# Performance work log

Hardware: AMD Instinct MI355X
Metric: run time of the kernel (lower is better)

The kernel has to match this reference:

```python
import jax, jax.numpy as jnp
import numpy as np


def setup_inputs() -> dict:
    key = jax.random.key(0)
    k1, k2, k3 = jax.random.split(key, 3)
    B, S, D = 8, 1024, 128
    logits = jax.random.normal(k1, (B, S, D), dtype=jnp.float32)
    labels = jax.random.normal(k2, (B, S, D), dtype=jnp.float32)
    # all-valid mask: any fully-padded row would make the softmax row all -inf (NaN),
    # matching the original torch behavior; ones keeps the baseline finite.
    pad_mask = jnp.ones((B, S), dtype=jnp.int32)
    ad_idxs = jax.random.randint(k3, (B, S), 0, 1000, dtype=jnp.int64)
    return {"logits": logits, "labels": labels, "pad_mask": pad_mask, "ad_idxs": ad_idxs}


def reference(logits, labels, pad_mask, ad_idxs):
    B, S, D = logits.shape
    N = B * S
    logits_flat = logits.reshape(N, D)
    labels_flat = labels.reshape(N, D)
    valid = pad_mask.reshape(N).astype(bool)
    ad = ad_idxs.reshape(N)

    # [N, N] pairwise similarity
    sim = logits_flat @ labels_flat.T
    pair_valid = valid[:, None] & valid[None, :]
    sim = jnp.where(pair_valid, sim, -jnp.inf)

    sim_prob = jax.nn.softmax(sim, axis=-1)

    label_mat = ((ad[:, None] == ad[None, :]) & pair_valid).astype(sim_prob.dtype)
    EPS = 1e-12
    pos_loss = -jnp.log2(jnp.clip(sim_prob, EPS)) * label_mat
    loss = pos_loss.sum(axis=-1).mean()
    return loss
```

## Files before the change

### kernel.cpp

```cpp
#include <hip/hip_runtime.h>
#include <math.h>

#define N 8192
#define D 128
#define NCHUNK 32
#define CHUNK_COLS (N / NCHUNK)
#define MAXPOS 32
#define NBUCKET 1000

#define CLIP_TERM 39.86313713864835f
#define LOG2E     1.4426950408889634f

typedef short bf16x8 __attribute__((ext_vector_type(8)));
typedef float f32x4  __attribute__((ext_vector_type(4)));

static __device__ __forceinline__ unsigned short f2bf(float f) {
    unsigned u = __builtin_bit_cast(unsigned, f);
    u += 0x7FFFu + ((u >> 16) & 1u);
    return (unsigned short)(u >> 16);
}

static __device__ __forceinline__ float exp2_fast(float x) {
    return __builtin_amdgcn_exp2f(x);
}

__global__ void convert_kernel(const float* __restrict__ a,
                               const float* __restrict__ b,
                               uint4* __restrict__ A,
                               uint4* __restrict__ B,
                               const int* __restrict__ ad,
                               int* __restrict__ bcnt,
                               int* __restrict__ blist,
                               int* __restrict__ cnt,
                               float* __restrict__ l_total,
                               float* __restrict__ out) {
    const int t = blockIdx.x * 256 + threadIdx.x;
    if (t < N) {
        cnt[t] = 0; l_total[t] = 0.0f;
        const int bv = ad[t];
        const int slot = atomicAdd(&bcnt[bv], 1);
        if (slot < MAXPOS) blist[bv * MAXPOS + slot] = t;
    }
    if (t == 0) *out = 0.0f;
    const int half = N * D / 8;
    const bool first = t < half;
    const int u = first ? t : t - half;
    const int r = u >> 4, k8 = u & 15;
    const float4* src = first ? (const float4*)a : (const float4*)b;
    float4 v0 = src[u * 2], v1 = src[u * 2 + 1];
    if (first) {
        v0.x *= LOG2E; v0.y *= LOG2E; v0.z *= LOG2E; v0.w *= LOG2E;
        v1.x *= LOG2E; v1.y *= LOG2E; v1.z *= LOG2E; v1.w *= LOG2E;
    }
    union { unsigned short us[8]; uint4 v; } p;
    p.us[0] = f2bf(v0.x); p.us[1] = f2bf(v0.y); p.us[2] = f2bf(v0.z); p.us[3] = f2bf(v0.w);
    p.us[4] = f2bf(v1.x); p.us[5] = f2bf(v1.y); p.us[6] = f2bf(v1.z); p.us[7] = f2bf(v1.w);
    const int chunk = ((r >> 4) * 4 + (k8 >> 2)) * 64 + (k8 & 3) * 16 + (r & 15);
    (first ? A : B)[chunk] = p.v;
}

__global__ __launch_bounds__(256, 2)
void sim_lse_kernel(const uint4* __restrict__ Ach,
                    const uint4* __restrict__ Bch,
                    float* __restrict__ l_total) {
    const int tid = threadIdx.x;
    const int lane = tid & 63;
    const int w = tid >> 6;
    const int quad = lane >> 4;
    const int rowBase = blockIdx.x * 256 + w * 64;
    const int col0 = blockIdx.y * CHUNK_COLS;
    const int rtile0 = rowBase >> 4;

    bf16x8 afr[4][4];
#pragma unroll
    for (int rt = 0; rt < 4; ++rt)
#pragma unroll
        for (int kt = 0; kt < 4; ++kt)
            afr[rt][kt] = __builtin_bit_cast(bf16x8,
                Ach[((rtile0 + rt) * 4 + kt) * 64 + lane]);

    float l[16];
#pragma unroll
    for (int s = 0; s < 16; ++s) l[s] = 0.0f;

#pragma unroll 2
    for (int cs = 0; cs < CHUNK_COLS / 32; ++cs) {
        const int ctile0 = (col0 >> 4) + cs * 2;

        bf16x8 bfr[2][4];
#pragma unroll
        for (int ct = 0; ct < 2; ++ct)
#pragma unroll
            for (int kt = 0; kt < 4; ++kt)
                bfr[ct][kt] = __builtin_bit_cast(bf16x8,
                    Bch[((ctile0 + ct) * 4 + kt) * 64 + lane]);

        f32x4 acc[4][2];
#pragma unroll
        for (int rt = 0; rt < 4; ++rt) { acc[rt][0] = (f32x4)(0.0f); acc[rt][1] = (f32x4)(0.0f); }

#pragma unroll
        for (int kt = 0; kt < 4; ++kt)
#pragma unroll
            for (int rt = 0; rt < 4; ++rt) {
                acc[rt][0] = __builtin_amdgcn_mfma_f32_16x16x32_bf16(afr[rt][kt], bfr[0][kt], acc[rt][0], 0, 0, 0);
                acc[rt][1] = __builtin_amdgcn_mfma_f32_16x16x32_bf16(afr[rt][kt], bfr[1][kt], acc[rt][1], 0, 0, 0);
            }

#pragma unroll
        for (int rt = 0; rt < 4; ++rt)
#pragma unroll
            for (int reg = 0; reg < 4; ++reg)
                l[rt * 4 + reg] += exp2_fast(acc[rt][0][reg]) + exp2_fast(acc[rt][1][reg]);
    }

#pragma unroll
    for (int s = 0; s < 16; ++s) {
        float ls = l[s];
#pragma unroll
        for (int off = 1; off < 16; off <<= 1) ls += __shfl_xor(ls, off, 64);
        if ((lane & 15) == 0) {
            const int rg = rowBase + (s >> 2) * 16 + quad * 4 + (s & 3);
            atomicAdd(&l_total[rg], ls);
        }
    }
}

__global__ __launch_bounds__(256)
void pos_pair_kernel(const float* __restrict__ logits,
                     const float* __restrict__ labels,
                     const int* __restrict__ bcnt,
                     const int* __restrict__ blist,
                     int* __restrict__ cnt,
                     float* __restrict__ pos_sim) {
    __shared__ float4 Lg[MAXPOS * 32];
    __shared__ float4 Lb[MAXPOS * 32];
    __shared__ int rows[MAXPOS];
    const int bId = blockIdx.x;
    const int nb = min(bcnt[bId], MAXPOS);
    const int tid = threadIdx.x;
    if (tid < nb) rows[tid] = blist[bId * MAXPOS + tid];
    __syncthreads();
    for (int idx = tid; idx < nb * 32; idx += 256) {
        const int rl = idx >> 5, c = idx & 31;
        const int rg = rows[rl];
        Lg[rl * 32 + c] = ((const float4*)logits)[rg * 32 + c];
        Lb[rl * 32 + c] = ((const float4*)labels)[rg * 32 + c];
    }
    __syncthreads();
    const int pairs = nb * nb;
    for (int p = tid; p < pairs; p += 256) {
        const int i = p / nb, j = p - i * nb;
        float sx = 0.f, sy = 0.f, sz = 0.f, sw = 0.f;
#pragma unroll 8
        for (int c = 0; c < 32; ++c) {
            const float4 x = Lg[i * 32 + c];
            const float4 y = Lb[j * 32 + c];
            sx = fmaf(x.x, y.x, sx); sy = fmaf(x.y, y.y, sy);
            sz = fmaf(x.z, y.z, sz); sw = fmaf(x.w, y.w, sw);
        }
        const float t = ((sx + sy) + (sz + sw)) * LOG2E;
        const int rg = rows[i];
        const int slot = atomicAdd(&cnt[rg], 1);
        if (slot < MAXPOS) pos_sim[rg * MAXPOS + slot] = t;
    }
}

__global__ __launch_bounds__(256)
void finalize_kernel(const float* __restrict__ l_total,
                     const int* __restrict__ cnt,
                     const float* __restrict__ pos_sim,
                     float* __restrict__ out) {
    const int i = blockIdx.x * 256 + threadIdx.x;
    const float lse = log2f(l_total[i]);
    const int n = min(cnt[i], MAXPOS);
    float sum = 0.0f;
    for (int k = 0; k < n; ++k)
        sum += fminf(lse - pos_sim[i * MAXPOS + k], CLIP_TERM);

#pragma unroll
    for (int off = 32; off >= 1; off >>= 1) sum += __shfl_xor(sum, off, 64);
    __shared__ float red[4];
    const int lane = threadIdx.x & 63, wid = threadIdx.x >> 6;
    if (lane == 0) red[wid] = sum;
    __syncthreads();
    if (threadIdx.x == 0)
        atomicAdd(out, (red[0] + red[1] + red[2] + red[3]) * (1.0f / (float)N));
}

extern "C" void kernel_launch(void* const* d_in, const int* in_sizes, int n_in,
                              void* d_out, int out_size, void* d_ws, size_t ws_size,
                              hipStream_t stream) {
    const float* logits = (const float*)d_in[0];
    const float* labels = (const float*)d_in[1];
    const int* ad = (const int*)d_in[3];
    float* out = (float*)d_out;

    uint4* Ach = (uint4*)d_ws;
    uint4* Bch = Ach + N * D / 8;
    float* l_total = (float*)(Bch + N * D / 8);
    int* cnt = (int*)(l_total + N);
    float* pos_sim = (float*)(cnt + N);
    int* bcnt = (int*)(pos_sim + N * MAXPOS);
    int* blist = bcnt + NBUCKET;

    hipMemsetAsync(bcnt, 0, NBUCKET * sizeof(int), stream);
    convert_kernel<<<2 * N * D / 8 / 256, 256, 0, stream>>>(
        logits, labels, Ach, Bch, ad, bcnt, blist, cnt, l_total, out);
    dim3 g(N / 256, NCHUNK);
    sim_lse_kernel<<<g, 256, 0, stream>>>(Ach, Bch, l_total);
    pos_pair_kernel<<<NBUCKET, 256, 0, stream>>>(logits, labels, bcnt, blist, cnt, pos_sim);
    finalize_kernel<<<N / 256, 256, 0, stream>>>(l_total, cnt, pos_sim, out);
}
```

Baseline: 107.0 us.

## Merge convert and positive-pair kernels, replace atomics with per-chunk partials

Folds the bf16 conversion and the positive-pair dot products into one prep kernel, where each bucket block scans all ad indices itself. This removes the memset, the bucket-list atomics and one kernel launch. The LSE accumulation switches from atomicAdd on l_total to writing per-chunk partial sums that finalize reduces. This avoids both atomic contention and the need to zero the buffer. In exchange, each of the 1000 bucket blocks reads the full 8192-entry index array, which adds redundant global reads.

Result: slower. 110.7 us (+3.4%).

```diff
diff --git a/kernel.cpp b/kernel.cpp
--- a/kernel.cpp
+++ b/kernel.cpp
@@ -24,123 +24,55 @@
     return __builtin_amdgcn_exp2f(x);
 }
 
-__global__ void convert_kernel(const float* __restrict__ a,
-                               const float* __restrict__ b,
-                               uint4* __restrict__ A,
-                               uint4* __restrict__ B,
-                               const int* __restrict__ ad,
-                               int* __restrict__ bcnt,
-                               int* __restrict__ blist,
-                               int* __restrict__ cnt,
-                               float* __restrict__ l_total,
-                               float* __restrict__ out) {
-    const int t = blockIdx.x * 256 + threadIdx.x;
-    if (t < N) {
-        cnt[t] = 0; l_total[t] = 0.0f;
-        const int bv = ad[t];
-        const int slot = atomicAdd(&bcnt[bv], 1);
-        if (slot < MAXPOS) blist[bv * MAXPOS + slot] = t;
-    }
-    if (t == 0) *out = 0.0f;
-    const int half = N * D / 8;
-    const bool first = t < half;
-    const int u = first ? t : t - half;
-    const int r = u >> 4, k8 = u & 15;
-    const float4* src = first ? (const float4*)a : (const float4*)b;
-    float4 v0 = src[u * 2], v1 = src[u * 2 + 1];
-    if (first) {
-        v0.x *= LOG2E; v0.y *= LOG2E; v0.z *= LOG2E; v0.w *= LOG2E;
-        v1.x *= LOG2E; v1.y *= LOG2E; v1.z *= LOG2E; v1.w *= LOG2E;
-    }
-    union { unsigned short us[8]; uint4 v; } p;
-    p.us[0] = f2bf(v0.x); p.us[1] = f2bf(v0.y); p.us[2] = f2bf(v0.z); p.us[3] = f2bf(v0.w);
-    p.us[4] = f2bf(v1.x); p.us[5] = f2bf(v1.y); p.us[6] = f2bf(v1.z); p.us[7] = f2bf(v1.w);
-    const int chunk = ((r >> 4) * 4 + (k8 >> 2)) * 64 + (k8 & 3) * 16 + (r & 15);
-    (first ? A : B)[chunk] = p.v;
-}
-
-__global__ __launch_bounds__(256, 2)
-void sim_lse_kernel(const uint4* __restrict__ Ach,
-                    const uint4* __restrict__ Bch,
-                    float* __restrict__ l_total) {
+__global__ __launch_bounds__(256)
+void prep_kernel(const float* __restrict__ logits,
+                 const float* __restrict__ labels,
+                 const int* __restrict__ ad,
+                 uint4* __restrict__ Ach,
+                 uint4* __restrict__ Bch,
+                 int* __restrict__ cnt,
+                 float* __restrict__ pos_sim,
+                 float* __restrict__ out) {
     const int tid = threadIdx.x;
-    const int lane = tid & 63;
-    const int w = tid >> 6;
-    const int quad = lane >> 4;
-    const int rowBase = blockIdx.x * 256 + w * 64;
-    const int col0 = blockIdx.y * CHUNK_COLS;
-    const int rtile0 = rowBase >> 4;
-
-    bf16x8 afr[4][4];
-#pragma unroll
-    for (int rt = 0; rt < 4; ++rt)
-#pragma unroll
-        for (int kt = 0; kt < 4; ++kt)
-            afr[rt][kt] = __builtin_bit_cast(bf16x8,
-                Ach[((rtile0 + rt) * 4 + kt) * 64 + lane]);
-
-    float l[16];
-#pragma unroll
-    for (int s = 0; s < 16; ++s) l[s] = 0.0f;
-
-#pragma unroll 2
-    for (int cs = 0; cs < CHUNK_COLS / 32; ++cs) {
-        const int ctile0 = (col0 >> 4) + cs * 2;
-
-        bf16x8 bfr[2][4];
-#pragma unroll
-        for (int ct = 0; ct < 2; ++ct)
-#pragma unroll
-            for (int kt = 0; kt < 4; ++kt)
-                bfr[ct][kt] = __builtin_bit_cast(bf16x8,
-                    Bch[((ctile0 + ct) * 4 + kt) * 64 + lane]);
-
-        f32x4 acc[4][2];
-#pragma unroll
-        for (int rt = 0; rt < 4; ++rt) { acc[rt][0] = (f32x4)(0.0f); acc[rt][1] = (f32x4)(0.0f); }
-
-#pragma unroll
-        for (int kt = 0; kt < 4; ++kt)
-#pragma unroll
-            for (int rt = 0; rt < 4; ++rt) {
-                acc[rt][0] = __builtin_amdgcn_mfma_f32_16x16x32_bf16(afr[rt][kt], bfr[0][kt], acc[rt][0], 0, 0, 0);
-                acc[rt][1] = __builtin_amdgcn_mfma_f32_16x16x32_bf16(afr[rt][kt], bfr[1][kt], acc[rt][1], 0, 0, 0);
-            }
-
-#pragma unroll
-        for (int rt = 0; rt < 4; ++rt)
-#pragma unroll
-            for (int reg = 0; reg < 4; ++reg)
-                l[rt * 4 + reg] += exp2_fast(acc[rt][0][reg]) + exp2_fast(acc[rt][1][reg]);
-    }
-
-#pragma unroll
-    for (int s = 0; s < 16; ++s) {
-        float ls = l[s];
-#pragma unroll
-        for (int off = 1; off < 16; off <<= 1) ls += __shfl_xor(ls, off, 64);
-        if ((lane & 15) == 0) {
-            const int rg = rowBase + (s >> 2) * 16 + quad * 4 + (s & 3);
-            atomicAdd(&l_total[rg], ls);
-        }
-    }
-}
-
-__global__ __launch_bounds__(256)
-void pos_pair_kernel(const float* __restrict__ logits,
-                     const float* __restrict__ labels,
-                     const int* __restrict__ bcnt,
-                     const int* __restrict__ blist,
-                     int* __restrict__ cnt,
-                     float* __restrict__ pos_sim) {
+
+    if (blockIdx.x < 2 * N * D / 8 / 256) {
+        const int t = blockIdx.x * 256 + tid;
+        if (t == 0) *out = 0.0f;
+        const int half = N * D / 8;
+        const bool first = t < half;
+        const int u = first ? t : t - half;
+        const int r = u >> 4, k8 = u & 15;
+        const float4* src = first ? (const float4*)logits : (const float4*)labels;
+        float4 v0 = src[u * 2], v1 = src[u * 2 + 1];
+        if (first) {
+            v0.x *= LOG2E; v0.y *= LOG2E; v0.z *= LOG2E; v0.w *= LOG2E;
+            v1.x *= LOG2E; v1.y *= LOG2E; v1.z *= LOG2E; v1.w *= LOG2E;
+        }
+        union { unsigned short us[8]; uint4 v; } p;
+        p.us[0] = f2bf(v0.x); p.us[1] = f2bf(v0.y); p.us[2] = f2bf(v0.z); p.us[3] = f2bf(v0.w);
+        p.us[4] = f2bf(v1.x); p.us[5] = f2bf(v1.y); p.us[6] = f2bf(v1.z); p.us[7] = f2bf(v1.w);
+        const int chunk = ((r >> 4) * 4 + (k8 >> 2)) * 64 + (k8 & 3) * 16 + (r & 15);
+        (first ? Ach : Bch)[chunk] = p.v;
+        return;
+    }
+
     __shared__ float4 Lg[MAXPOS * 32];
     __shared__ float4 Lb[MAXPOS * 32];
     __shared__ int rows[MAXPOS];
-    const int bId = blockIdx.x;
-    const int nb = min(bcnt[bId], MAXPOS);
-    const int tid = threadIdx.x;
-    if (tid < nb) rows[tid] = blist[bId * MAXPOS + tid];
-    __syncthreads();
+    __shared__ int nbs;
+    const int bId = blockIdx.x - 2 * N * D / 8 / 256;
+    if (tid == 0) nbs = 0;
+    __syncthreads();
+    for (int r = tid; r < N; r += 256) {
+        if (ad[r] == bId) {
+            const int s = atomicAdd(&nbs, 1);
+            if (s < MAXPOS) rows[s] = r;
+            else cnt[r] = 0;
+        }
+    }
+    __syncthreads();
+    const int nb = min(nbs, MAXPOS);
+    if (tid < nb) cnt[rows[tid]] = nb;
     for (int idx = tid; idx < nb * 32; idx += 256) {
         const int rl = idx >> 5, c = idx & 31;
         const int rg = rows[rl];
@@ -159,20 +91,91 @@
             sx = fmaf(x.x, y.x, sx); sy = fmaf(x.y, y.y, sy);
             sz = fmaf(x.z, y.z, sz); sw = fmaf(x.w, y.w, sw);
         }
-        const float t = ((sx + sy) + (sz + sw)) * LOG2E;
-        const int rg = rows[i];
-        const int slot = atomicAdd(&cnt[rg], 1);
-        if (slot < MAXPOS) pos_sim[rg * MAXPOS + slot] = t;
+        pos_sim[rows[i] * MAXPOS + j] = ((sx + sy) + (sz + sw)) * LOG2E;
+    }
+}
+
+__global__ __launch_bounds__(256, 2)
+void sim_lse_kernel(const uint4* __restrict__ Ach,
+                    const uint4* __restrict__ Bch,
+                    float* __restrict__ partial) {
+    const int tid = threadIdx.x;
+    const int lane = tid & 63;
+    const int w = tid >> 6;
+    const int quad = lane >> 4;
+    const int rowBase = blockIdx.x * 256 + w * 64;
+    const int col0 = blockIdx.y * CHUNK_COLS;
+    const int rtile0 = rowBase >> 4;
+
+    bf16x8 afr[4][4];
+#pragma unroll
+    for (int rt = 0; rt < 4; ++rt)
+#pragma unroll
+        for (int kt = 0; kt < 4; ++kt)
+            afr[rt][kt] = __builtin_bit_cast(bf16x8,
+                Ach[((rtile0 + rt) * 4 + kt) * 64 + lane]);
+
+    float l[16];
+#pragma unroll
+    for (int s = 0; s < 16; ++s) l[s] = 0.0f;
+
+#pragma unroll 2
+    for (int cs = 0; cs < CHUNK_COLS / 32; ++cs) {
+        const int ctile0 = (col0 >> 4) + cs * 2;
+
+        bf16x8 bfr[2][4];
+#pragma unroll
+        for (int ct = 0; ct < 2; ++ct)
+#pragma unroll
+            for (int kt = 0; kt < 4; ++kt)
+                bfr[ct][kt] = __builtin_bit_cast(bf16x8,
+                    Bch[((ctile0 + ct) * 4 + kt) * 64 + lane]);
+
+        f32x4 acc[4][2];
+#pragma unroll
+        for (int rt = 0; rt < 4; ++rt) { acc[rt][0] = (f32x4)(0.0f); acc[rt][1] = (f32x4)(0.0f); }
+
+#pragma unroll
+        for (int kt = 0; kt < 4; ++kt)
+#pragma unroll
+            for (int rt = 0; rt < 4; ++rt) {
+                acc[rt][0] = __builtin_amdgcn_mfma_f32_16x16x32_bf16(afr[rt][kt], bfr[0][kt], acc[rt][0], 0, 0, 0);
+                acc[rt][1] = __builtin_amdgcn_mfma_f32_16x16x32_bf16(afr[rt][kt], bfr[1][kt], acc[rt][1], 0, 0, 0);
+            }
+
+#pragma unroll
+        for (int rt = 0; rt < 4; ++rt)
+#pragma unroll
+            for (int reg = 0; reg < 4; ++reg)
+                l[rt * 4 + reg] += exp2_fast(acc[rt][0][reg]) + exp2_fast(acc[rt][1][reg]);
+    }
+
+#pragma unroll
+    for (int s = 0; s < 16; ++s) {
+        float ls = l[s];
+#pragma unroll
+        for (int off = 1; off < 16; off <<= 1) ls += __shfl_xor(ls, off, 64);
+        if ((lane & 15) == 0) {
+            const int rg = rowBase + (s >> 2) * 16 + quad * 4 + (s & 3);
+            partial[rg * NCHUNK + blockIdx.y] = ls;
+        }
     }
 }
 
 __global__ __launch_bounds__(256)
-void finalize_kernel(const float* __restrict__ l_total,
+void finalize_kernel(const float* __restrict__ partial,
                      const int* __restrict__ cnt,
                      const float* __restrict__ pos_sim,
                      float* __restrict__ out) {
     const int i = blockIdx.x * 256 + threadIdx.x;
-    const float lse = log2f(l_total[i]);
+    const float4* pp = (const float4*)(partial + i * NCHUNK);
+    float s0 = 0.f, s1 = 0.f, s2 = 0.f, s3 = 0.f;
+#pragma unroll
+    for (int q = 0; q < NCHUNK / 4; ++q) {
+        const float4 v = pp[q];
+        s0 += v.x; s1 += v.y; s2 += v.z; s3 += v.w;
+    }
+    const float lse = log2f((s0 + s1) + (s2 + s3));
     const int n = min(cnt[i], MAXPOS);
     float sum = 0.0f;
     for (int k = 0; k < n; ++k)
@@ -198,17 +201,13 @@
 
     uint4* Ach = (uint4*)d_ws;
     uint4* Bch = Ach + N * D / 8;
-    float* l_total = (float*)(Bch + N * D / 8);
-    int* cnt = (int*)(l_total + N);
+    float* partial = (float*)(Bch + N * D / 8);
+    int* cnt = (int*)(partial + N * NCHUNK);
     float* pos_sim = (float*)(cnt + N);
-    int* bcnt = (int*)(pos_sim + N * MAXPOS);
-    int* blist = bcnt + NBUCKET;
-
-    hipMemsetAsync(bcnt, 0, NBUCKET * sizeof(int), stream);
-    convert_kernel<<<2 * N * D / 8 / 256, 256, 0, stream>>>(
-        logits, labels, Ach, Bch, ad, bcnt, blist, cnt, l_total, out);
+
+    prep_kernel<<<2 * N * D / 8 / 256 + NBUCKET, 256, 0, stream>>>(
+        logits, labels, ad, Ach, Bch, cnt, pos_sim, out);
     dim3 g(N / 256, NCHUNK);
-    sim_lse_kernel<<<g, 256, 0, stream>>>(Ach, Bch, l_total);
-    pos_pair_kernel<<<NBUCKET, 256, 0, stream>>>(logits, labels, bcnt, blist, cnt, pos_sim);
-    finalize_kernel<<<N / 256, 256, 0, stream>>>(l_total, cnt, pos_sim, out);
-}
+    sim_lse_kernel<<<g, 256, 0, stream>>>(Ach, Bch, partial);
+    finalize_kernel<<<N / 256, 256, 0, stream>>>(partial, cnt, pos_sim, out);
+}
```
